# Performance work log

Hardware: AMD Instinct MI355X
Metric: run time of the kernel (lower is better)

Reference implementation:

```python
import jax, jax.numpy as jnp
import numpy as np

K, S, P, NQ, NREPS = 3, 1, 1, 9, 2  # kernel, stride, pad, num_qubits, num_qreps


def _extract_patches(x, k, s):
    # x: (b, c, H, W) -> (b, c, ho, wo, k*k), patch elems in (kh, kw) row-major order
    b, c, H, W = x.shape
    ho = (H - k) // s + 1
    wo = (W - k) // s + 1
    cols = [x[:, :, i:i + (ho - 1) * s + 1:s, j:j + (wo - 1) * s + 1:s]
            for i in range(k) for j in range(k)]
    return jnp.stack(cols, axis=-1), ho, wo


def _cnot(state, c, t):
    # state: (N, 2, ..., 2); CNOT with control wire c, target wire t (wire q -> axis q+1)
    s0, s1 = jnp.split(state, 2, axis=c + 1)
    return jnp.concatenate([s0, jnp.flip(s1, axis=t + 1)], axis=c + 1)


def _simulate(angles, weights):
    # AngleEmbedding(RX) + BasicEntanglerLayers(RZ, CNOT ring) + expval(PauliY_i)
    # angles: (N, n) float; weights: (L, n) float -> (N, n) float expvals
    N, n = angles.shape
    half = 0.5 * angles
    # RX(theta)|0> = cos(t/2)|0> - i sin(t/2)|1>  (product state)
    vecs = jnp.stack([jnp.cos(half).astype(jnp.complex64),
                      -1j * jnp.sin(half)], axis=-1)  # (N, n, 2)
    state = vecs[:, 0]
    for q in range(1, n):
        state = state[..., None] * vecs[:, q].reshape((N,) + (1,) * q + (2,))
    # state: (N, 2, ..., 2), wire 0 = axis 1 (most significant)
    for l in range(weights.shape[0]):
        # RZ layer = single diagonal of shape (2,)*n, shared across patches
        pv = jnp.stack([jnp.exp(-0.5j * weights[l]),
                        jnp.exp(0.5j * weights[l])], axis=-1).astype(jnp.complex64)  # (n,2)
        diag = pv[0]
        for q in range(1, n):
            diag = diag[..., None] * pv[q].reshape((1,) * q + (2,))
        state = state * diag
        # CNOT ring (i -> i+1 mod n), as in BasicEntanglerLayers for n > 2
        for i in range(n):
            state = _cnot(state, i, (i + 1) % n)
    # <Y_i> = 2 * Im( sum conj(psi_{qi=0}) * psi_{qi=1} )
    exps = []
    for i in range(n):
        a, bdim = 1 << i, 1 << (n - 1 - i)
        r = state.reshape(N, a, 2, bdim)
        z = jnp.sum(jnp.conj(r[:, :, 0, :]) * r[:, :, 1, :], axis=(1, 2))
        exps.append(2.0 * z.imag)
    return jnp.stack(exps, axis=1)  # (N, n) float32


def setup_inputs() -> dict:
    key = jax.random.key(0)
    k1, k2 = jax.random.split(key)
    x = jax.random.uniform(k1, (16, 1, 28, 28), dtype=jnp.float32)
    weights = jax.random.uniform(k2, (NREPS, NQ), dtype=jnp.float32,
                                 minval=0.0, maxval=2.0 * np.pi)
    return {"x": x, "weights": weights}


def reference(x, weights):
    b = x.shape[0]
    xp = jnp.pad(x, ((0, 0), (0, 0), (P, P), (P, P)))
    patches, ho, wo = _extract_patches(xp, K, S)  # (b, 1, ho, wo, k*k)
    flat = patches.reshape(-1, NQ)                # (b*ho*wo, 9)  (c == 1)
    qout = _simulate(flat, weights)               # (b*ho*wo, 9)
    qout = qout.reshape(b, ho, wo, NQ)
    return qout.transpose(0, 3, 1, 2)             # (b, 9, ho, wo)
```

## Files before the change

### kernel.cpp

```cpp
#include <hip/hip_runtime.h>
#include <math.h>

#define NQ 9
#define NREPS 2
#define NB 512
#define NSIMS (16*28*28)

__host__ __device__ constexpr int csigma(int b) {
    for (int c = NQ - 1; c >= 0; --c) {
        const int t  = (c + 1) % NQ;
        const int pc = NQ - 1 - c;
        const int pt = NQ - 1 - t;
        b ^= ((b >> pc) & 1) << pt;
    }
    return b;
}
__host__ __device__ constexpr int csig2(int b) { return csigma(csigma(b)); }

__host__ __device__ constexpr int PIOF(int i)  { return NQ - 1 - i; }
__host__ __device__ constexpr int VMASK(int i) { return csig2(1 << PIOF(i)); }
__host__ __device__ constexpr int SCOMP(int i) { return (~VMASK(i)) & ((1 << NQ) - 1); }
__host__ __device__ constexpr int NV(int i)    { int m = SCOMP(i), c = 0; while (m) { c += m & 1; m >>= 1; } return c; }
__host__ __device__ constexpr int POSI(int i, int t) {
    int m = SCOMP(i), p = 0;
    while (true) { if (m & 1) { if (t == 0) return p; --t; } m >>= 1; ++p; }
}

constexpr int COLC[NQ] = {
    csig2(1 << 0), csig2(1 << 1), csig2(1 << 2), csig2(1 << 3), csig2(1 << 4),
    csig2(1 << 5), csig2(1 << 6), csig2(1 << 7), csig2(1 << 8)
};

template<int L>
__device__ __forceinline__ float heval(const float* __restrict__ cf, const float* vx) {
    if constexpr (L == 2) {
        const float4 g = *reinterpret_cast<const float4*>(cf);
        return (g.x + vx[0] * g.y) + vx[1] * (g.z + vx[0] * g.w);
    } else {
        return heval<L - 1>(cf, vx) + vx[L - 1] * heval<L - 1>(cf + (1 << (L - 1)), vx);
    }
}

template<int I>
__device__ __forceinline__ float qubit_eval(const float* __restrict__ coefI,
                                            const float* ca, const float* sa) {
    constexpr int V = NV(I);
    float vx[7];
    if constexpr (V > 0) vx[0] = ca[NQ - 1 - POSI(I, 0)];
    if constexpr (V > 1) vx[1] = ca[NQ - 1 - POSI(I, 1)];
    if constexpr (V > 2) vx[2] = ca[NQ - 1 - POSI(I, 2)];
    if constexpr (V > 3) vx[3] = ca[NQ - 1 - POSI(I, 3)];
    if constexpr (V > 4) vx[4] = ca[NQ - 1 - POSI(I, 4)];
    if constexpr (V > 5) vx[5] = ca[NQ - 1 - POSI(I, 5)];
    if constexpr (V > 6) vx[6] = ca[NQ - 1 - POSI(I, 6)];
    const float g = heval<V>(coefI, vx);
    float sp = 1.f;
    if constexpr ((VMASK(I) & (1 << 0)) != 0) sp *= sa[8];
    if constexpr ((VMASK(I) & (1 << 1)) != 0) sp *= sa[7];
    if constexpr ((VMASK(I) & (1 << 2)) != 0) sp *= sa[6];
    if constexpr ((VMASK(I) & (1 << 3)) != 0) sp *= sa[5];
    if constexpr ((VMASK(I) & (1 << 4)) != 0) sp *= sa[4];
    if constexpr ((VMASK(I) & (1 << 5)) != 0) sp *= sa[3];
    if constexpr ((VMASK(I) & (1 << 6)) != 0) sp *= sa[2];
    if constexpr ((VMASK(I) & (1 << 7)) != 0) sp *= sa[1];
    if constexpr ((VMASK(I) & (1 << 8)) != 0) sp *= sa[0];
    return sp * g;
}

template<int I>
__device__ __forceinline__ void qubit_block(
    const float* __restrict__ x, float* __restrict__ out,
    const float* sTc, const float* sTs, float* sD, float* sCoef,
    const int tid, const int bx)
{
    constexpr int Pi  = NQ - 1 - I;
    constexpr int NVI = NV(I);

    {
        const int y  = tid;
        const int b  = ((y >> Pi) << (Pi + 1)) | (y & ((1 << Pi) - 1));
        const int b2 = b | (1 << Pi);
        sD[y] = sTs[b2] * sTc[b] - sTc[b2] * sTs[b];
    }
    __syncthreads();

    #pragma unroll
    for (int s = 0; s < 8; ++s) {
        if (tid < 128) {
            const int k  = tid;
            const int y0 = ((k >> s) << (s + 1)) | (k & ((1 << s) - 1));
            const int y1 = y0 | (1 << s);
            const float a = sD[y0], bb = sD[y1];
            sD[y0] = a + bb;
            sD[y1] = a - bb;
        }
        __syncthreads();
    }

    if (tid < (1 << NVI)) {
        const int u = tid;
        int sc = SCOMP(I), J = 0, uu = u;
        while (sc) { const int low = sc & (-sc); if (uu & 1) J |= low; sc &= sc - 1; uu >>= 1; }
        int MJ = 0;
        #pragma unroll
        for (int k = 0; k < NQ; ++k) MJ |= (__popc((unsigned)(COLC[k] & J)) & 1) << k;
        const int w8 = ((MJ >> (Pi + 1)) << Pi) | (MJ & ((1 << Pi) - 1));
        sCoef[u] = sD[w8] * (1.0f / 256.0f);
    }
    __syncthreads();

    const int sim = bx * 256 + tid;
    const int ox  = sim % 28;
    const int t1  = sim / 28;
    const int oy  = t1 % 28;
    const int img = t1 / 28;

    float ca[NQ], sa[NQ];
    #pragma unroll
    for (int q = 0; q < NQ; ++q) {
        const int ky = q / 3, kx = q % 3;
        const int yy = oy + ky - 1, xx = ox + kx - 1;
        float a = 0.f;
        if (yy >= 0 && yy < 28 && xx >= 0 && xx < 28)
            a = x[img * 784 + yy * 28 + xx];
        __sincosf(a, &sa[q], &ca[q]);
    }

    out[img * (NQ * 784) + I * 784 + oy * 28 + ox] = qubit_eval<I>(sCoef, ca, sa);
}

__global__ __launch_bounds__(256) void quanv_fused(
    const float* __restrict__ x,
    const float* __restrict__ w,
    float* __restrict__ out)
{
    __shared__ float sTc[NB], sTs[NB];
    __shared__ float sD[256];
    __shared__ __align__(16) float sCoef[128];
    const int tid = threadIdx.x;

    #pragma unroll
    for (int b0 = 0; b0 < NB; b0 += 256) {
        const int b = b0 + tid;
        float th = 0.f;
        int cur = b;
        #pragma unroll
        for (int l = NREPS - 1; l >= 0; --l) {
            cur = csigma(cur);
            #pragma unroll
            for (int q = 0; q < NQ; ++q) {
                const float wq = 0.5f * w[l * NQ + q];
                th += ((cur >> (NQ - 1 - q)) & 1) ? wq : -wq;
            }
        }
        th -= 1.5707963267948966f * (float)__popc((unsigned)cur);
        float s, c;
        sincosf(th, &s, &c);
        sTc[b] = c; sTs[b] = s;
    }
    __syncthreads();

    switch (blockIdx.y) {
        case 0: qubit_block<0>(x, out, sTc, sTs, sD, sCoef, tid, blockIdx.x); break;
        case 1: qubit_block<1>(x, out, sTc, sTs, sD, sCoef, tid, blockIdx.x); break;
        case 2: qubit_block<2>(x, out, sTc, sTs, sD, sCoef, tid, blockIdx.x); break;
        case 3: qubit_block<3>(x, out, sTc, sTs, sD, sCoef, tid, blockIdx.x); break;
        case 4: qubit_block<4>(x, out, sTc, sTs, sD, sCoef, tid, blockIdx.x); break;
        case 5: qubit_block<5>(x, out, sTc, sTs, sD, sCoef, tid, blockIdx.x); break;
        case 6: qubit_block<6>(x, out, sTc, sTs, sD, sCoef, tid, blockIdx.x); break;
        case 7: qubit_block<7>(x, out, sTc, sTs, sD, sCoef, tid, blockIdx.x); break;
        case 8: qubit_block<8>(x, out, sTc, sTs, sD, sCoef, tid, blockIdx.x); break;
    }
}

extern "C" void kernel_launch(void* const* d_in, const int* in_sizes, int n_in,
                              void* d_out, int out_size, void* d_ws, size_t ws_size,
                              hipStream_t stream) {
    const float* x = (const float*)d_in[0];
    const float* w = (const float*)d_in[1];
    float* out = (float*)d_out;
    (void)d_ws; (void)ws_size; (void)in_sizes; (void)n_in; (void)out_size;

    quanv_fused<<<dim3(NSIMS / 256, NQ), 256, 0, stream>>>(x, w, out);
}
```

Baseline: 60.51 us.

## Run per-qubit Walsh-Hadamard transform in registers with one wave per block

Blocks shrink from 256 to 64 threads (one wavefront), and the grid grows fourfold. Each lane now holds four of the 256 values and runs the 8-stage Walsh-Hadamard butterfly with DPP, ds_swizzle and shuffle lane exchanges plus two in-register stages. This replaces the shared-memory butterflies and their barrier after every stage. The coefficient gather now uses a precomputed constexpr inverse table instead of computing parity per thread, and the phase table moves to float2 with fast __sincosf. The cost is that each smaller block recomputes the 512-entry phase table, so that work is now repeated four times as often.

```diff
diff --git a/kernel.cpp b/kernel.cpp
--- a/kernel.cpp
+++ b/kernel.cpp
@@ -30,6 +30,49 @@
     csig2(1 << 0), csig2(1 << 1), csig2(1 << 2), csig2(1 << 3), csig2(1 << 4),
     csig2(1 << 5), csig2(1 << 6), csig2(1 << 7), csig2(1 << 8)
 };
+
+struct InvTab { unsigned short v[NQ][256]; };
+__host__ __device__ constexpr InvTab make_inv() {
+    InvTab t{};
+    for (int i = 0; i < NQ; ++i)
+        for (int y = 0; y < 256; ++y) t.v[i][y] = 0xFFFF;
+    for (int i = 0; i < NQ; ++i) {
+        const int Pi = NQ - 1 - i;
+        for (int u = 0; u < (1 << NV(i)); ++u) {
+            int sc = SCOMP(i), J = 0, uu = u;
+            while (sc) { const int low = sc & (-sc); if (uu & 1) J |= low; sc &= sc - 1; uu >>= 1; }
+            int MJ = 0;
+            for (int k = 0; k < NQ; ++k) {
+                int x = COLC[k] & J, p = 0;
+                while (x) { p ^= x & 1; x >>= 1; }
+                MJ |= p << k;
+            }
+            const int w8 = ((MJ >> (Pi + 1)) << Pi) | (MJ & ((1 << Pi) - 1));
+            t.v[i][w8] = (unsigned short)u;
+        }
+    }
+    return t;
+}
+__device__ constexpr InvTab INVTAB = make_inv();
+
+template<int CTRL>
+__device__ __forceinline__ float dppmov(float x) {
+    return __int_as_float(__builtin_amdgcn_update_dpp(
+        0, __float_as_int(x), CTRL, 0xF, 0xF, true));
+}
+template<int OFF>
+__device__ __forceinline__ float swzx(float x) {
+    return __int_as_float(__builtin_amdgcn_ds_swizzle(__float_as_int(x), OFF));
+}
+template<int P>
+__device__ __forceinline__ float lane_xor(float x) {
+    if constexpr (P == 0) return dppmov<0xB1>(x);
+    else if constexpr (P == 1) return dppmov<0x4E>(x);
+    else if constexpr (P == 2) return swzx<0x101F>(x);
+    else if constexpr (P == 3) return dppmov<0x128>(x);
+    else if constexpr (P == 4) return swzx<0x401F>(x);
+    else return __shfl_xor(x, 32, 64);
+}
 
 template<int L>
 __device__ __forceinline__ float heval(const float* __restrict__ cf, const float* vx) {
@@ -67,49 +110,59 @@
     return sp * g;
 }
 
+#define WHT_STAGE(S)                                              \
+    {                                                             \
+        const float sg = ((lane >> (S)) & 1) ? -1.f : 1.f;        \
+        const float p0 = lane_xor<S>(r0);                         \
+        const float p1 = lane_xor<S>(r1);                         \
+        const float p2 = lane_xor<S>(r2);                         \
+        const float p3 = lane_xor<S>(r3);                         \
+        r0 = fmaf(sg, r0, p0);                                    \
+        r1 = fmaf(sg, r1, p1);                                    \
+        r2 = fmaf(sg, r2, p2);                                    \
+        r3 = fmaf(sg, r3, p3);                                    \
+    }
+
 template<int I>
 __device__ __forceinline__ void qubit_block(
     const float* __restrict__ x, float* __restrict__ out,
-    const float* sTc, const float* sTs, float* sD, float* sCoef,
-    const int tid, const int bx)
+    const float2* sT2, float* sCoef, const int lane, const int bx)
 {
-    constexpr int Pi  = NQ - 1 - I;
-    constexpr int NVI = NV(I);
-
+    constexpr int Pi = NQ - 1 - I;
+
+    float r0, r1, r2, r3;
     {
-        const int y  = tid;
-        const int b  = ((y >> Pi) << (Pi + 1)) | (y & ((1 << Pi) - 1));
-        const int b2 = b | (1 << Pi);
-        sD[y] = sTs[b2] * sTc[b] - sTc[b2] * sTs[b];
-    }
+        float* rr[1]; (void)rr;
+        #define LOAD_D(K, DST)                                                        \
+        {                                                                             \
+            const int y  = ((K) << 6) | lane;                                         \
+            const int b  = ((y >> Pi) << (Pi + 1)) | (y & ((1 << Pi) - 1));           \
+            const int b2 = b | (1 << Pi);                                             \
+            const float2 A = sT2[b];                                                  \
+            const float2 B = sT2[b2];                                                 \
+            DST = B.y * A.x - B.x * A.y;                                              \
+        }
+        LOAD_D(0, r0) LOAD_D(1, r1) LOAD_D(2, r2) LOAD_D(3, r3)
+        #undef LOAD_D
+    }
+
+    WHT_STAGE(0) WHT_STAGE(1) WHT_STAGE(2) WHT_STAGE(3) WHT_STAGE(4) WHT_STAGE(5)
+    {
+        const float t0 = r0 + r1, t1 = r0 - r1, t2 = r2 + r3, t3 = r2 - r3;
+        r0 = t0 + t2; r2 = t0 - t2; r1 = t1 + t3; r3 = t1 - t3;
+    }
+
+    #define STORE_C(K, SRC)                                                  \
+    {                                                                        \
+        const int y = ((K) << 6) | lane;                                     \
+        const unsigned short u = INVTAB.v[I][y];                             \
+        if (u != 0xFFFF) sCoef[u] = (SRC) * (1.0f / 256.0f);                 \
+    }
+    STORE_C(0, r0) STORE_C(1, r1) STORE_C(2, r2) STORE_C(3, r3)
+    #undef STORE_C
     __syncthreads();
 
-    #pragma unroll
-    for (int s = 0; s < 8; ++s) {
-        if (tid < 128) {
-            const int k  = tid;
-            const int y0 = ((k >> s) << (s + 1)) | (k & ((1 << s) - 1));
-            const int y1 = y0 | (1 << s);
-            const float a = sD[y0], bb = sD[y1];
-            sD[y0] = a + bb;
-            sD[y1] = a - bb;
-        }
-        __syncthreads();
-    }
-
-    if (tid < (1 << NVI)) {
-        const int u = tid;
-        int sc = SCOMP(I), J = 0, uu = u;
-        while (sc) { const int low = sc & (-sc); if (uu & 1) J |= low; sc &= sc - 1; uu >>= 1; }
-        int MJ = 0;
-        #pragma unroll
-        for (int k = 0; k < NQ; ++k) MJ |= (__popc((unsigned)(COLC[k] & J)) & 1) << k;
-        const int w8 = ((MJ >> (Pi + 1)) << Pi) | (MJ & ((1 << Pi) - 1));
-        sCoef[u] = sD[w8] * (1.0f / 256.0f);
-    }
-    __syncthreads();
-
-    const int sim = bx * 256 + tid;
+    const int sim = bx * 64 + lane;
     const int ox  = sim % 28;
     const int t1  = sim / 28;
     const int oy  = t1 % 28;
@@ -129,19 +182,18 @@
     out[img * (NQ * 784) + I * 784 + oy * 28 + ox] = qubit_eval<I>(sCoef, ca, sa);
 }
 
-__global__ __launch_bounds__(256) void quanv_fused(
+__global__ __launch_bounds__(64) void quanv_fused(
     const float* __restrict__ x,
     const float* __restrict__ w,
     float* __restrict__ out)
 {
-    __shared__ float sTc[NB], sTs[NB];
-    __shared__ float sD[256];
+    __shared__ float2 sT2[NB];
     __shared__ __align__(16) float sCoef[128];
-    const int tid = threadIdx.x;
+    const int lane = threadIdx.x;
 
     #pragma unroll
-    for (int b0 = 0; b0 < NB; b0 += 256) {
-        const int b = b0 + tid;
+    for (int k8 = 0; k8 < 8; ++k8) {
+        const int b = k8 * 64 + lane;
         float th = 0.f;
         int cur = b;
         #pragma unroll
@@ -155,21 +207,21 @@
         }
         th -= 1.5707963267948966f * (float)__popc((unsigned)cur);
         float s, c;
-        sincosf(th, &s, &c);
-        sTc[b] = c; sTs[b] = s;
+        __sincosf(th, &s, &c);
+        sT2[b] = make_float2(c, s);
     }
     __syncthreads();
 
     switch (blockIdx.y) {
-        case 0: qubit_block<0>(x, out, sTc, sTs, sD, sCoef, tid, blockIdx.x); break;
-        case 1: qubit_block<1>(x, out, sTc, sTs, sD, sCoef, tid, blockIdx.x); break;
-        case 2: qubit_block<2>(x, out, sTc, sTs, sD, sCoef, tid, blockIdx.x); break;
-        case 3: qubit_block<3>(x, out, sTc, sTs, sD, sCoef, tid, blockIdx.x); break;
-        case 4: qubit_block<4>(x, out, sTc, sTs, sD, sCoef, tid, blockIdx.x); break;
-        case 5: qubit_block<5>(x, out, sTc, sTs, sD, sCoef, tid, blockIdx.x); break;
-        case 6: qubit_block<6>(x, out, sTc, sTs, sD, sCoef, tid, blockIdx.x); break;
-        case 7: qubit_block<7>(x, out, sTc, sTs, sD, sCoef, tid, blockIdx.x); break;
-        case 8: qubit_block<8>(x, out, sTc, sTs, sD, sCoef, tid, blockIdx.x); break;
+        case 0: qubit_block<0>(x, out, sT2, sCoef, lane, blockIdx.x); break;
+        case 1: qubit_block<1>(x, out, sT2, sCoef, lane, blockIdx.x); break;
+        case 2: qubit_block<2>(x, out, sT2, sCoef, lane, blockIdx.x); break;
+        case 3: qubit_block<3>(x, out, sT2, sCoef, lane, blockIdx.x); break;
+        case 4: qubit_block<4>(x, out, sT2, sCoef, lane, blockIdx.x); break;
+        case 5: qubit_block<5>(x, out, sT2, sCoef, lane, blockIdx.x); break;
+        case 6: qubit_block<6>(x, out, sT2, sCoef, lane, blockIdx.x); break;
+        case 7: qubit_block<7>(x, out, sT2, sCoef, lane, blockIdx.x); break;
+        case 8: qubit_block<8>(x, out, sT2, sCoef, lane, blockIdx.x); break;
     }
 }
 
@@ -181,5 +233,5 @@
     float* out = (float*)d_out;
     (void)d_ws; (void)ws_size; (void)in_sizes; (void)n_in; (void)out_size;
 
-    quanv_fused<<<dim3(NSIMS / 256, NQ), 256, 0, stream>>>(x, w, out);
-}
+    quanv_fused<<<dim3(NSIMS / 64, NQ), 64, 0, stream>>>(x, w, out);
+}
```

Result: slower. 62.76 us (+3.7%).
